# Kernel optimization log

Measured on AMD Instinct MI355X. Metric: run time of the kernel, lower is better.

## Reference

```python
import jax, jax.numpy as jnp
import numpy as np

EPS = 1e-6
R_DEPTH = 12   # CONFIG['max_recursion_depth']
STACK = 48     # CONFIG['stack_size']
GB, CG, CC = 0.8, 2.0, 0.25  # graph_bias_scale, context_gate_strength, commitment_cost


def _g(k, shape, s=0.05):
    return (jax.random.normal(k, shape) * s).astype(jnp.float32)


def setup_inputs():
    D, V, B, S = 128, 16384, 32, 128
    NS, NM = 64, 128
    ks = iter(jax.random.split(jax.random.key(0), 40))
    return {
        "input_ids": jax.random.randint(next(ks), (B, S), 0, V),
        "prev_syn_idx": jax.random.randint(next(ks), (B,), 0, NS),
        "prev_sem_idx": jax.random.randint(next(ks), (B,), 0, NM),
        "emb_mag": _g(next(ks), (V, D), 1.0),
        "emb_phase": _g(next(ks), (V, D), 1.0),
        "cell_Wr": _g(next(ks), (D, D)), "cell_Wi": _g(next(ks), (D, D)),
        "norm_scale": jnp.ones((D,), jnp.float32),
        "norm_shift": jnp.zeros((D,), jnp.float32),
        "modrelu_b": jnp.zeros((D,), jnp.float32),
        "qWr": _g(next(ks), (D, D)), "qWi": _g(next(ks), (D, D)),
        "kWr": _g(next(ks), (D, D)), "kWi": _g(next(ks), (D, D)),
        "vWr": _g(next(ks), (D, D)), "vWi": _g(next(ks), (D, D)),
        "oWr": _g(next(ks), (D, D)), "oWi": _g(next(ks), (D, D)),
        "halt_W": _g(next(ks), (2 * D, 1)),
        "halt_b": jnp.full((1,), -2.0, jnp.float32),  # nn.init.constant_(halt_linear.bias, -2.0)
        "stk_W": _g(next(ks), (2 * D, 3)), "stk_b": jnp.zeros((3,), jnp.float32),
        "cb_syn": _g(next(ks), (64, 2 * D), 1.0),
        "cb_sem": _g(next(ks), (128, 2 * D), 1.0),
        "ctxsyn_W": _g(next(ks), (2 * D, NS)), "ctxsyn_b": jnp.zeros((NS,), jnp.float32),
        "ctxsem_W": _g(next(ks), (2 * D, NM)), "ctxsem_b": jnp.zeros((NM,), jnp.float32),
        "adj_syn": _g(next(ks), (NS, NS), 1.0),
        "adj_sem": _g(next(ks), (NM, NM), 1.0),
        "gate_W": _g(next(ks), (4 * D, D)), "gate_b": jnp.zeros((D,), jnp.float32),
        "dec_W": _g(next(ks), (2 * D, V)), "dec_b": jnp.zeros((V,), jnp.float32),
    }


def _forward(fl, input_ids, prev_syn_idx, prev_sem_idx):
    (emb_mag, emb_phase, cell_Wr, cell_Wi, norm_scale, norm_shift, modrelu_b,
     qWr, qWi, kWr, kWi, vWr, vWi, oWr, oWi, halt_W, halt_b, stk_W, stk_b,
     cb_syn, cb_sem, ctxsyn_W, ctxsyn_b, ctxsem_W, ctxsem_b, adj_syn, adj_sem,
     gate_W, gate_b, dec_W, dec_b) = fl
    B = input_ids.shape[0]
    D = emb_mag.shape[1]
    sg = jax.lax.stop_gradient

    def clin(r, i, Wr, Wi):  # ComplexLinear (no bias)
        return r @ Wr - i @ Wi, i @ Wr + r @ Wi

    def cell(zr, zi):  # AdaptiveRecursiveCell
        r, i = clin(zr, zi, cell_Wr, cell_Wi)
        # ComplexLayerNorm (torch.var is unbiased -> ddof=1)
        mag = jnp.sqrt(r * r + i * i) + EPS
        mean = mag.mean(-1, keepdims=True)
        var = jnp.var(mag, axis=-1, ddof=1, keepdims=True)
        nm = (mag - mean) / jnp.sqrt(var + EPS) * norm_scale + norm_shift
        r, i = nm * r / mag, nm * i / mag  # cos/sin of original phase
        # ModReLU
        n = jnp.sqrt(r * r + i * i) + EPS
        s = jax.nn.relu(n + modrelu_b) / n
        r, i = r * s, i * s
        # MultiHeadComplexAttention: source computes Q,K but out = V -> o_proj(v_proj(z))
        vr, vi = clin(r, i, vWr, vWi)
        r, i = clin(vr, vi, oWr, oWi)
        zf = jnp.concatenate([r, i], -1)
        halt = jax.nn.sigmoid(zf @ halt_W + halt_b)          # [B,1]
        ctrl = jax.nn.softmax(zf @ stk_W + stk_b, axis=-1)   # [B,3]
        return r, i, halt, ctrl

    def stack_step(zr, zi, mem, ptr, ctrl):  # DifferentiableStack
        push, pop, noop = ctrl[:, 0:1], ctrl[:, 1:2], ctrl[:, 2:3]
        pu, pd = jnp.roll(ptr, 1, axis=1), jnp.roll(ptr, -1, axis=1)
        nptr = push * pu + pop * pd + noop * ptr
        nptr = nptr / (nptr.sum(1, keepdims=True) + EPS)
        zf = jnp.concatenate([zr, zi], -1)
        wm = (push * pu)[:, :, None]                          # write mask [B,STACK,1]
        mem = wm * zf[:, None, :] + mem * (1.0 - wm)
        read = (mem * nptr[:, :, None]).sum(1)                # [B,2D]
        return read[:, :D], read[:, D:], mem, nptr

    def gres(zr, zi, sr, si):  # GatedResidual, g_c = g + i*g
        g = jax.nn.sigmoid(jnp.concatenate([zr, zi, sr, si], -1) @ gate_W + gate_b)
        return ((1.0 - g) * zr + g * zi + g * (sr - si),
                (1.0 - g) * zi - g * zr + g * (si + sr))

    def vq(zr, zi, cb, adj, cW, cbias, pidx):  # ContextAwareDualVQ.vq_step (eval mode)
        zf = jnp.concatenate([zr, zi], -1)                    # [B,2D]
        d = (zf * zf).sum(1, keepdims=True) + (cb * cb).sum(1) - 2.0 * zf @ cb.T
        d = d - GB * jax.nn.sigmoid(adj[pidx]) - CG * jax.nn.softmax(zf @ cW + cbias, -1)
        idx = jnp.argmin(d, axis=1)
        zq = cb[idx]
        loss = jnp.mean((sg(zq) - zf) ** 2) + CC * jnp.mean((zq - sg(zf)) ** 2)
        return zf + sg(zq - zf), loss, idx                    # STE

    def step(carry, ids_t):
        mem, ptr, psyn, psem, lacc = carry
        r, th = emb_mag[ids_t], emb_phase[ids_t]              # embed
        zr, zi = r * jnp.cos(th), r * jnp.sin(th)
        rem = jnp.ones((B, 1), zr.dtype)
        accr = jnp.zeros_like(zr); acci = jnp.zeros_like(zi)
        slr = jnp.zeros_like(zr); sli = jnp.zeros_like(zi)
        for n in range(R_DEPTH):  # ACT recursion, halting-weighted accumulation
            pr, pi, halt, ctrl = cell(zr, zi)
            rr, ri, mem, ptr = stack_step(pr, pi, mem, ptr, ctrl)
            zr, zi = gres(pr, pi, rr, ri)
            w = rem if n == R_DEPTH - 1 else rem * halt
            accr, acci = accr + w * zr, acci + w * zi
            rem = rem * (1.0 - halt)
            slr, sli = slr + zr / R_DEPTH, sli + zi / R_DEPTH
        zqs, ls, isyn = vq(accr, acci, cb_syn, adj_syn, ctxsyn_W, ctxsyn_b, psyn)
        zqm, lm, isem = vq(slr, sli, cb_sem, adj_sem, ctxsem_W, ctxsem_b, psem)
        logits = 0.5 * (zqs + zqm) @ dec_W + dec_b            # decoder: Linear(2D, V)
        return (mem, ptr, isyn, isem, lacc + ls + lm), logits

    mem0 = jnp.zeros((B, STACK, 2 * D), jnp.float32)
    ptr0 = jnp.zeros((B, STACK), jnp.float32).at[:, 0].set(1.0)
    carry0 = (mem0, ptr0, prev_syn_idx, prev_sem_idx, jnp.zeros((), jnp.float32))
    (_, _, _, _, vq_loss), logits = jax.lax.scan(step, carry0, input_ids.T)
    return jnp.transpose(logits, (1, 0, 2)), vq_loss          # [B,S,V], scalar


def reference(input_ids, prev_syn_idx, prev_sem_idx, emb_mag, emb_phase, cell_Wr, cell_Wi, norm_scale, norm_shift, modrelu_b, qWr, qWi, kWr, kWi, vWr, vWi, oWr, oWi, halt_W, halt_b, stk_W, stk_b, cb_syn, cb_sem, ctxsyn_W, ctxsyn_b, ctxsem_W, ctxsem_b, adj_syn, adj_sem, gate_W, gate_b, dec_W, dec_b):
    fl = (emb_mag, emb_phase, cell_Wr, cell_Wi, norm_scale, norm_shift, modrelu_b,
          qWr, qWi, kWr, kWi, vWr, vWi, oWr, oWi, halt_W, halt_b, stk_W, stk_b,
          cb_syn, cb_sem, ctxsyn_W, ctxsyn_b, ctxsem_W, ctxsem_b, adj_syn, adj_sem,
          gate_W, gate_b, dec_W, dec_b)
    return _forward(fl, input_ids, prev_syn_idx, prev_sem_idx)
```

## Files before the change

kernel.cpp:

```cpp
#include <hip/hip_runtime.h>
#include <math.h>

#define D 128
#define D2 256
#define STK 48
#define SEQ 128
#define BATCH 32
#define RDPT 12
#define NSYN 64
#define NSEM 128
#define VOC 16384
#define EPSF 1e-6f
#define GB_C 0.8f
#define CG_C 2.0f

struct RParams {
  const int* input_ids;
  const int* prev_syn;
  const int* prev_sem;
  const float* emb_mag;
  const float* emb_phase;
  const float* cell_Wr;
  const float* cell_Wi;
  const float* norm_scale;
  const float* norm_shift;
  const float* modrelu_b;
  const float* VOr;
  const float* VOi;
  const float* halt_W;
  const float* halt_b;
  const float* stk_W;
  const float* stk_b;
  const float* cb_syn;
  const float* cb_sem;
  const float* ctxsyn_W;
  const float* ctxsyn_b;
  const float* ctxsem_W;
  const float* ctxsem_b;
  const float* gate_W;
  const float* gate_b;
  const float* cbT_syn;
  const float* cbT_sem;
  const float* cnrm_syn;
  const float* cnrm_sem;
  const float* gbsig_syn;
  const float* gbsig_sem;
  float* X;
  float* lossp;
};

__device__ __forceinline__ float waveAllSum(float v) {
  #pragma unroll
  for (int m = 32; m; m >>= 1) v += __shfl_xor(v, m);
  return v;
}

__global__ __launch_bounds__(512, 2) void recur_kernel(RParams p) {
  __shared__ float4 VO4[(D / 2) * D];
  __shared__ float partr[512], parti[512];
  __shared__ alignas(16) float xr_[D], xi_[D], cr_[D], ci_[D];
  __shared__ alignas(16) float zfc[D2], rd_[D2];
  __shared__ alignas(16) float acc2[D2], sl2[D2];
  __shared__ float zqs[D2];
  __shared__ float sptr[STK];
  __shared__ alignas(16) float nptrs[STK], wms[STK];
  __shared__ float sns_s[D], nsh_s[D], smb_s[D];
  __shared__ float hW_s[D2];
  __shared__ float stW_s[D2 * 3];
  __shared__ float scal[16];
  __shared__ int icb[2];
  __shared__ int ids[SEQ];

  const int tid = threadIdx.x;
  const int b = blockIdx.x;
  const int l = tid & 63;
  const int j = tid & 127;
  const int kq = tid >> 7;
  const int k0 = kq * 32;

  float cwr[32], cwi[32];
  #pragma unroll
  for (int kk = 0; kk < 32; ++kk) {
    cwr[kk] = p.cell_Wr[(size_t)(k0 + kk) * D + j];
    cwi[kk] = p.cell_Wi[(size_t)(k0 + kk) * D + j];
  }
  float gw[128];
  #pragma unroll
  for (int kk = 0; kk < 128; ++kk)
    gw[kk] = p.gate_W[(size_t)(kq * 128 + kk) * D + j];
  for (int e = tid; e < (D / 2) * D; e += 512) {
    const int kp = e >> 7;
    const int jj = e & 127;
    float4 w;
    w.x = p.VOr[(size_t)(2 * kp) * D + jj];
    w.y = p.VOi[(size_t)(2 * kp) * D + jj];
    w.z = p.VOr[(size_t)(2 * kp + 1) * D + jj];
    w.w = p.VOi[(size_t)(2 * kp + 1) * D + jj];
    VO4[e] = w;
  }
  if (tid < D) {
    sns_s[tid] = p.norm_scale[tid];
    nsh_s[tid] = p.norm_shift[tid];
    smb_s[tid] = p.modrelu_b[tid];
  }
  const float sgbR = (tid < D) ? p.gate_b[tid] : 0.f;
  if (tid < D2) hW_s[tid] = p.halt_W[tid];
  for (int e = tid; e < D2 * 3; e += 512) stW_s[e] = p.stk_W[e];
  if (tid < SEQ) ids[tid] = p.input_ids[(size_t)b * SEQ + tid];
  if (tid < STK) sptr[tid] = (tid == 0) ? 1.f : 0.f;
  if (tid == 0) { icb[0] = p.prev_syn[b]; icb[1] = p.prev_sem[b]; }
  const float hb = p.halt_b[0];
  const float sb0 = p.stk_b[0], sb1 = p.stk_b[1], sb2 = p.stk_b[2];

  float memv[24];
  #pragma unroll
  for (int q = 0; q < 24; ++q) memv[q] = 0.f;
  const int mdl = tid & 255, mjh = tid >> 8;
  float lossAcc = 0.f;
  float remv = 1.f;
  float mNxt = 0.f, pNxt = 0.f;
  __syncthreads();

  if (tid < D) {
    const int id0 = ids[0];
    mNxt = p.emb_mag[(size_t)id0 * D + tid];
    pNxt = p.emb_phase[(size_t)id0 * D + tid];
  }

  for (int t = 0; t < SEQ; ++t) {
    if (tid < D) {
      float sv, cv;
      sincosf(pNxt, &sv, &cv);
      xr_[tid] = mNxt * cv;
      xi_[tid] = mNxt * sv;
    }
    float accR = 0.f, accI = 0.f, slR = 0.f, slI = 0.f;
    if (tid < 64) remv = 1.f;
    __syncthreads();

    for (int n = 0; n < RDPT; ++n) {
      {
        const float4* x4r = (const float4*)(&xr_[k0]);
        const float4* x4i = (const float4*)(&xi_[k0]);
        float a0 = 0.f, a1 = 0.f, a2 = 0.f, a3 = 0.f;
        #pragma unroll
        for (int q = 0; q < 8; ++q) {
          float4 xa = x4r[q];
          float4 xb = x4i[q];
          a0 = fmaf(xa.x, cwr[q*4+0], a0); a0 = fmaf(-xb.x, cwi[q*4+0], a0);
          a1 = fmaf(xb.x, cwr[q*4+0], a1); a1 = fmaf(xa.x, cwi[q*4+0], a1);
          a2 = fmaf(xa.y, cwr[q*4+1], a2); a2 = fmaf(-xb.y, cwi[q*4+1], a2);
          a3 = fmaf(xb.y, cwr[q*4+1], a3); a3 = fmaf(xa.y, cwi[q*4+1], a3);
          a0 = fmaf(xa.z, cwr[q*4+2], a0); a0 = fmaf(-xb.z, cwi[q*4+2], a0);
          a1 = fmaf(xb.z, cwr[q*4+2], a1); a1 = fmaf(xa.z, cwi[q*4+2], a1);
          a2 = fmaf(xa.w, cwr[q*4+3], a2); a2 = fmaf(-xb.w, cwi[q*4+3], a2);
          a3 = fmaf(xb.w, cwr[q*4+3], a3); a3 = fmaf(xa.w, cwi[q*4+3], a3);
        }
        partr[tid] = a0 + a2;
        parti[tid] = a1 + a3;
      }
      __syncthreads();
      if (tid < 64) {
        float rr0 = 0.f, ii0 = 0.f, rr1 = 0.f, ii1 = 0.f;
        #pragma unroll
        for (int q = 0; q < 4; ++q) {
          rr0 += partr[l + q * 128];       ii0 += parti[l + q * 128];
          rr1 += partr[l + 64 + q * 128];  ii1 += parti[l + 64 + q * 128];
        }
        float m0 = sqrtf(rr0 * rr0 + ii0 * ii0) + EPSF;
        float m1 = sqrtf(rr1 * rr1 + ii1 * ii1) + EPSF;
        float mean = waveAllSum(m0 + m1) * (1.f / D);
        float dd0 = m0 - mean, dd1 = m1 - mean;
        float istd = rsqrtf(waveAllSum(dd0 * dd0 + dd1 * dd1) * (1.f / (D - 1)) + EPSF);
        float nm0 = (m0 - mean) * istd * sns_s[l] + nsh_s[l];
        float r0_ = nm0 * rr0 / m0, i0_ = nm0 * ii0 / m0;
        float nn0 = sqrtf(r0_ * r0_ + i0_ * i0_) + EPSF;
        float sc0 = fmaxf(nn0 + smb_s[l], 0.f) / nn0;
        cr_[l] = r0_ * sc0;
        ci_[l] = i0_ * sc0;
        float nm1 = (m1 - mean) * istd * sns_s[l + 64] + nsh_s[l + 64];
        float r1_ = nm1 * rr1 / m1, i1_ = nm1 * ii1 / m1;
        float nn1 = sqrtf(r1_ * r1_ + i1_ * i1_) + EPSF;
        float sc1 = fmaxf(nn1 + smb_s[l + 64], 0.f) / nn1;
        cr_[l + 64] = r1_ * sc1;
        ci_[l + 64] = i1_ * sc1;
      }
      __syncthreads();
      {
        const float4* c4r = (const float4*)(&cr_[k0]);
        const float4* c4i = (const float4*)(&ci_[k0]);
        const float4* vbase = &VO4[(size_t)(k0 >> 1) * D + j];
        float a0 = 0.f, a1 = 0.f, a2 = 0.f, a3 = 0.f;
        #pragma unroll
        for (int q = 0; q < 8; ++q) {
          float4 xa = c4r[q];
          float4 xb = c4i[q];
          float4 wA = vbase[(size_t)(2 * q) * D];
          float4 wB = vbase[(size_t)(2 * q + 1) * D];
          a0 = fmaf(xa.x, wA.x, a0); a0 = fmaf(-xb.x, wA.y, a0);
          a1 = fmaf(xb.x, wA.x, a1); a1 = fmaf(xa.x, wA.y, a1);
          a2 = fmaf(xa.y, wA.z, a2); a2 = fmaf(-xb.y, wA.w, a2);
          a3 = fmaf(xb.y, wA.z, a3); a3 = fmaf(xa.y, wA.w, a3);
          a0 = fmaf(xa.z, wB.x, a0); a0 = fmaf(-xb.z, wB.y, a0);
          a1 = fmaf(xb.z, wB.x, a1); a1 = fmaf(xa.z, wB.y, a1);
          a2 = fmaf(xa.w, wB.z, a2); a2 = fmaf(-xb.w, wB.w, a2);
          a3 = fmaf(xb.w, wB.z, a3); a3 = fmaf(xa.w, wB.w, a3);
        }
        partr[tid] = a0 + a2;
        parti[tid] = a1 + a3;
      }
      __syncthreads();
      if (tid < 256) {
        if (tid < 128) {
          zfc[tid] = partr[tid] + partr[tid + 128] + partr[tid + 256] + partr[tid + 384];
        } else {
          const int d = tid - 128;
          zfc[tid] = parti[d] + parti[d + 128] + parti[d + 256] + parti[d + 384];
        }
      }
      __syncthreads();
      if (tid < 64) {
        float z0 = zfc[l], z1 = zfc[l + 64], z2 = zfc[l + 128], z3 = zfc[l + 192];
        float dh  = z0 * hW_s[l] + z1 * hW_s[l + 64] + z2 * hW_s[l + 128] + z3 * hW_s[l + 192];
        float dc0 = z0 * stW_s[l * 3 + 0] + z1 * stW_s[(l + 64) * 3 + 0] +
                    z2 * stW_s[(l + 128) * 3 + 0] + z3 * stW_s[(l + 192) * 3 + 0];
        float dc1 = z0 * stW_s[l * 3 + 1] + z1 * stW_s[(l + 64) * 3 + 1] +
                    z2 * stW_s[(l + 128) * 3 + 1] + z3 * stW_s[(l + 192) * 3 + 1];
        float dc2 = z0 * stW_s[l * 3 + 2] + z1 * stW_s[(l + 64) * 3 + 2] +
                    z2 * stW_s[(l + 128) * 3 + 2] + z3 * stW_s[(l + 192) * 3 + 2];
        dh = waveAllSum(dh);
        dc0 = waveAllSum(dc0);
        dc1 = waveAllSum(dc1);
        dc2 = waveAllSum(dc2);
        float halt = 1.f / (1.f + expf(-(dh + hb)));
        float e0 = dc0 + sb0, e1 = dc1 + sb1, e2 = dc2 + sb2;
        float mx = fmaxf(e0, fmaxf(e1, e2));
        float x0 = expf(e0 - mx), x1 = expf(e1 - mx), x2 = expf(e2 - mx);
        float sm = x0 + x1 + x2;
        float push = x0 / sm, pop = x1 / sm, noop = x2 / sm;
        float wgt = (n == RDPT - 1) ? remv : remv * halt;
        if (l == 0) scal[3] = wgt;
        remv = remv * (1.f - halt);
        float pj = 0.f, pu = 0.f, pd = 0.f;
        if (l < STK) {
          pj = sptr[l];
          pu = sptr[(l + STK - 1) % STK];
          pd = sptr[(l + 1) % STK];
        }
        float np_ = push * pu + pop * pd + noop * pj;
        float wm_ = push * pu;
        float ssum = waveAllSum((l < STK) ? np_ : 0.f);
        float inv = 1.f / (ssum + EPSF);
        if (l < STK) {
          np_ *= inv;
          nptrs[l] = np_;
          sptr[l] = np_;
          wms[l] = wm_;
        }
      }
      __syncthreads();
      {
        const float4* wm4 = (const float4*)wms;
        const float4* np4 = (const float4*)nptrs;
        float zfd = zfc[mdl];
        float accA = 0.f, accB = 0.f;
        #pragma unroll
        for (int m4 = 0; m4 < 6; ++m4) {
          float4 wmv = wm4[mjh * 6 + m4];
          float4 npv = np4[mjh * 6 + m4];
          const int base = m4 * 4;
          memv[base + 0] = wmv.x * zfd + memv[base + 0] * (1.f - wmv.x);
          accA = fmaf(memv[base + 0], npv.x, accA);
          memv[base + 1] = wmv.y * zfd + memv[base + 1] * (1.f - wmv.y);
          accB = fmaf(memv[base + 1], npv.y, accB);
          memv[base + 2] = wmv.z * zfd + memv[base + 2] * (1.f - wmv.z);
          accA = fmaf(memv[base + 2], npv.z, accA);
          memv[base + 3] = wmv.w * zfd + memv[base + 3] * (1.f - wmv.w);
          accB = fmaf(memv[base + 3], npv.w, accB);
        }
        partr[tid] = accA + accB;
      }
      __syncthreads();
      if (tid < D2) rd_[tid] = partr[tid] + partr[tid + 256];
      __syncthreads();
      {
        const float4* src4 = (kq < 2) ? (const float4*)(&zfc[kq * 128])
                                      : (const float4*)(&rd_[(kq - 2) * 128]);
        float g0 = 0.f, g1 = 0.f, g2 = 0.f, g3 = 0.f;
        #pragma unroll
        for (int q = 0; q < 32; ++q) {
          float4 xv = src4[q];
          g0 = fmaf(xv.x, gw[q * 4 + 0], g0);
          g1 = fmaf(xv.y, gw[q * 4 + 1], g1);
          g2 = fmaf(xv.z, gw[q * 4 + 2], g2);
          g3 = fmaf(xv.w, gw[q * 4 + 3], g3);
        }
        partr[tid] = (g0 + g1) + (g2 + g3);
      }
      __syncthreads();
      if (tid < D) {
        float g = partr[tid] + partr[tid + 128] + partr[tid + 256] +
                  partr[tid + 384] + sgbR;
        g = 1.f / (1.f + expf(-g));
        float pr_ = zfc[tid], pi_ = zfc[tid + 128];
        float rr_ = rd_[tid], ri_ = rd_[tid + 128];
        float nzr = (1.f - g) * pr_ + g * pi_ + g * (rr_ - ri_);
        float nzi = (1.f - g) * pi_ - g * pr_ + g * (ri_ + rr_);
        xr_[tid] = nzr;
        xi_[tid] = nzi;
        float wgt = scal[3];
        accR += wgt * nzr;
        accI += wgt * nzi;
        slR += nzr * (1.f / RDPT);
        slI += nzi * (1.f / RDPT);
      }
      __syncthreads();
    }

    if (tid < D) {
      const int idn = ids[(t + 1 < SEQ) ? t + 1 : t];
      mNxt = p.emb_mag[(size_t)idn * D + tid];
      pNxt = p.emb_phase[(size_t)idn * D + tid];
    }
    if (tid < D) {
      acc2[tid] = accR; acc2[tid + 128] = accI;
      sl2[tid] = slR;  sl2[tid + 128] = slI;
    }
    __syncthreads();

    {
      const int c = tid & 63, ch = tid >> 6;
      const int kb = ch * 32;
      const float* cb = p.cbT_syn + (size_t)kb * 64 + c;
      const float* cw = p.ctxsyn_W + (size_t)kb * 64 + c;
      const float4* a4 = (const float4*)(&acc2[kb]);
      float d0 = 0.f, d1 = 0.f, e0 = 0.f, e1 = 0.f;
      #pragma unroll
      for (int q = 0; q < 8; ++q) {
        float4 zv = a4[q];
        d0 = fmaf(cb[(size_t)(q * 4 + 0) * 64], zv.x, d0);
        e0 = fmaf(cw[(size_t)(q * 4 + 0) * 64], zv.x, e0);
        d1 = fmaf(cb[(size_t)(q * 4 + 1) * 64], zv.y, d1);
        e1 = fmaf(cw[(size_t)(q * 4 + 1) * 64], zv.y, e1);
        d0 = fmaf(cb[(size_t)(q * 4 + 2) * 64], zv.z, d0);
        e0 = fmaf(cw[(size_t)(q * 4 + 2) * 64], zv.z, e0);
        d1 = fmaf(cb[(size_t)(q * 4 + 3) * 64], zv.w, d1);
        e1 = fmaf(cw[(size_t)(q * 4 + 3) * 64], zv.w, e1);
      }
      partr[ch * 64 + c] = d0 + d1;
      parti[ch * 64 + c] = e0 + e1;
    }
    __syncthreads();
    if (tid < 64) {
      float dot = 0.f, e = p.ctxsyn_b[l];
      #pragma unroll
      for (int ch = 0; ch < 8; ++ch) {
        dot += partr[ch * 64 + l];
        e += parti[ch * 64 + l];
      }
      float d = p.cnrm_syn[l] - 2.f * dot;
      float m = e;
      #pragma unroll
      for (int mm = 32; mm; mm >>= 1) m = fmaxf(m, __shfl_xor(m, mm));
      float ex = expf(e - m);
      float s = waveAllSum(ex);
      const int pidx = icb[0];
      float score = d - p.gbsig_syn[(size_t)pidx * 64 + l] - CG_C * (ex / s);
      float bv = score; int bi = l;
      #pragma unroll
      for (int mm = 32; mm; mm >>= 1) {
        float ov = __shfl_xor(bv, mm); int oi = __shfl_xor(bi, mm);
        if (ov < bv || (ov == bv && oi < bi)) { bv = ov; bi = oi; }
      }
      if (l == 0) icb[0] = bi;
    }
    __syncthreads();
    if (tid < D2) {
      const int idx = icb[0];
      float zqv = p.cb_syn[(size_t)idx * D2 + tid];
      float df = zqv - acc2[tid];
      lossAcc += df * df;
      zqs[tid] = zqv;
    }
    {
      const int c = tid & 127, ch = tid >> 7;
      const int kb = ch * 64;
      const float* cb = p.cbT_sem + (size_t)kb * 128 + c;
      const float* cw = p.ctxsem_W + (size_t)kb * 128 + c;
      const float4* a4 = (const float4*)(&sl2[kb]);
      float d0 = 0.f, d1 = 0.f, e0 = 0.f, e1 = 0.f;
      #pragma unroll
      for (int q = 0; q < 16; ++q) {
        float4 zv = a4[q];
        d0 = fmaf(cb[(size_t)(q * 4 + 0) * 128], zv.x, d0);
        e0 = fmaf(cw[(size_t)(q * 4 + 0) * 128], zv.x, e0);
        d1 = fmaf(cb[(size_t)(q * 4 + 1) * 128], zv.y, d1);
        e1 = fmaf(cw[(size_t)(q * 4 + 1) * 128], zv.y, e1);
        d0 = fmaf(cb[(size_t)(q * 4 + 2) * 128], zv.z, d0);
        e0 = fmaf(cw[(size_t)(q * 4 + 2) * 128], zv.z, e0);
        d1 = fmaf(cb[(size_t)(q * 4 + 3) * 128], zv.w, d1);
        e1 = fmaf(cw[(size_t)(q * 4 + 3) * 128], zv.w, e1);
      }
      partr[ch * 128 + c] = d0 + d1;
      parti[ch * 128 + c] = e0 + e1;
    }
    __syncthreads();
    if (tid < 64) {
      float dot0 = 0.f, e0 = p.ctxsem_b[l];
      float dot1 = 0.f, e1 = p.ctxsem_b[l + 64];
      #pragma unroll
      for (int ch = 0; ch < 4; ++ch) {
        dot0 += partr[ch * 128 + l];       e0 += parti[ch * 128 + l];
        dot1 += partr[ch * 128 + l + 64];  e1 += parti[ch * 128 + l + 64];
      }
      float d0 = p.cnrm_sem[l] - 2.f * dot0;
      float d1 = p.cnrm_sem[l + 64] - 2.f * dot1;
      float m = fmaxf(e0, e1);
      #pragma unroll
      for (int mm = 32; mm; mm >>= 1) m = fmaxf(m, __shfl_xor(m, mm));
      float x0 = expf(e0 - m), x1 = expf(e1 - m);
      float s = waveAllSum(x0 + x1);
      const int pidx = icb[1];
      float s0 = d0 - p.gbsig_sem[(size_t)pidx * 128 + l] - CG_C * (x0 / s);
      float s1 = d1 - p.gbsig_sem[(size_t)pidx * 128 + l + 64] - CG_C * (x1 / s);
      float bv = s0; int bi = l;
      if (s1 < bv) { bv = s1; bi = l + 64; }
      #pragma unroll
      for (int mm = 32; mm; mm >>= 1) {
        float ov = __shfl_xor(bv, mm); int oi = __shfl_xor(bi, mm);
        if (ov < bv || (ov == bv && oi < bi)) { bv = ov; bi = oi; }
      }
      if (l == 0) icb[1] = bi;
    }
    __syncthreads();
    if (tid < D2) {
      const int idx = icb[1];
      float zqv = p.cb_sem[(size_t)idx * D2 + tid];
      float df = zqv - sl2[tid];
      lossAcc += df * df;
      p.X[(size_t)(b * SEQ + t) * D2 + tid] = 0.5f * (zqs[tid] + zqv);
    }
    __syncthreads();
  }

  partr[tid] = lossAcc;
  __syncthreads();
  if (tid < 256) partr[tid] += partr[tid + 256];
  __syncthreads();
  if (tid < 128) partr[tid] += partr[tid + 128];
  __syncthreads();
  if (tid < 64) {
    float v = partr[tid] + partr[tid + 64];
    v = waveAllSum(v);
    if (tid == 0) p.lossp[b] = v;
  }
}

__global__ __launch_bounds__(256) void voprod_kernel(const float* __restrict__ vr,
                                                     const float* __restrict__ vi,
                                                     const float* __restrict__ orr,
                                                     const float* __restrict__ oii,
                                                     float* __restrict__ VOr,
                                                     float* __restrict__ VOi) {
  __shared__ float a_r[D], a_i[D];
  const int k = blockIdx.x;
  const int tid = threadIdx.x;
  if (tid < D) { a_r[tid] = vr[k * D + tid]; a_i[tid] = vi[k * D + tid]; }
  __syncthreads();
  const int m = tid & 127;
  const int half = tid >> 7;
  float acc = 0.f;
  if (half == 0) {
    #pragma unroll 8
    for (int jj = 0; jj < D; ++jj)
      acc += a_r[jj] * orr[jj * D + m] - a_i[jj] * oii[jj * D + m];
    VOr[k * D + m] = acc;
  } else {
    #pragma unroll 8
    for (int jj = 0; jj < D; ++jj)
      acc += a_r[jj] * oii[jj * D + m] + a_i[jj] * orr[jj * D + m];
    VOi[k * D + m] = acc;
  }
}

__global__ void vqprep_kernel(const float* __restrict__ cb_syn,
                              const float* __restrict__ cb_sem,
                              const float* __restrict__ adj_syn,
                              const float* __restrict__ adj_sem,
                              float* __restrict__ cbT_syn,
                              float* __restrict__ cbT_sem,
                              float* __restrict__ cnrm_syn,
                              float* __restrict__ cnrm_sem,
                              float* __restrict__ gbsig_syn,
                              float* __restrict__ gbsig_sem) {
  const int tid = blockIdx.x * 256 + threadIdx.x;
  const int nt = gridDim.x * 256;
  for (int e = tid; e < NSYN * D2; e += nt) {
    int c = e / D2, k = e % D2;
    cbT_syn[k * NSYN + c] = cb_syn[e];
  }
  for (int e = tid; e < NSEM * D2; e += nt) {
    int c = e / D2, k = e % D2;
    cbT_sem[k * NSEM + c] = cb_sem[e];
  }
  for (int c = tid; c < NSYN; c += nt) {
    float s = 0.f;
    for (int k = 0; k < D2; ++k) { float v = cb_syn[c * D2 + k]; s += v * v; }
    cnrm_syn[c] = s;
  }
  for (int c = tid; c < NSEM; c += nt) {
    float s = 0.f;
    for (int k = 0; k < D2; ++k) { float v = cb_sem[c * D2 + k]; s += v * v; }
    cnrm_sem[c] = s;
  }
  for (int e = tid; e < NSYN * NSYN; e += nt)
    gbsig_syn[e] = GB_C / (1.f + expf(-adj_syn[e]));
  for (int e = tid; e < NSEM * NSEM; e += nt)
    gbsig_sem[e] = GB_C / (1.f + expf(-adj_sem[e]));
}

__global__ __launch_bounds__(256) void dec_kernel(const float* __restrict__ X,
                                                  const float* __restrict__ W,
                                                  const float* __restrict__ bias,
                                                  float* __restrict__ out) {
  __shared__ float A[32][D2];
  const int tid = threadIdx.x;
  const int bx = blockIdx.x;
  const int by = blockIdx.y;
  const float* xr = X + (size_t)by * 32 * D2;
  #pragma unroll
  for (int s = 0; s < 32; ++s) A[s][tid] = xr[s * D2 + tid];
  __syncthreads();
  const int ty = tid >> 5, tx = tid & 31;
  const int col0 = bx * 128 + tx * 4;
  const int r0 = ty * 4;
  float acc[4][4];
  #pragma unroll
  for (int r = 0; r < 4; ++r) {
    acc[r][0] = 0.f; acc[r][1] = 0.f; acc[r][2] = 0.f; acc[r][3] = 0.f;
  }
  const float* wp = W + col0;
  for (int k = 0; k < D2; k += 4) {
    float4 w0 = *(const float4*)(wp + (size_t)(k + 0) * VOC);
    float4 w1 = *(const float4*)(wp + (size_t)(k + 1) * VOC);
    float4 w2 = *(const float4*)(wp + (size_t)(k + 2) * VOC);
    float4 w3 = *(const float4*)(wp + (size_t)(k + 3) * VOC);
    #pragma unroll
    for (int r = 0; r < 4; ++r) {
      float4 a = *(const float4*)&A[r0 + r][k];
      acc[r][0] += a.x * w0.x + a.y * w1.x + a.z * w2.x + a.w * w3.x;
      acc[r][1] += a.x * w0.y + a.y * w1.y + a.z * w2.y + a.w * w3.y;
      acc[r][2] += a.x * w0.z + a.y * w1.z + a.z * w2.z + a.w * w3.z;
      acc[r][3] += a.x * w0.w + a.y * w1.w + a.z * w2.w + a.w * w3.w;
    }
  }
  float4 bv = *(const float4*)(bias + col0);
  #pragma unroll
  for (int r = 0; r < 4; ++r) {
    float4 o;
    o.x = acc[r][0] + bv.x; o.y = acc[r][1] + bv.y;
    o.z = acc[r][2] + bv.z; o.w = acc[r][3] + bv.w;
    *(float4*)(out + (size_t)(by * 32 + r0 + r) * VOC + col0) = o;
  }
}

__global__ void loss_kernel(const float* __restrict__ lp, float* __restrict__ out) {
  int l = threadIdx.x;
  float v = (l < BATCH) ? lp[l] : 0.f;
  #pragma unroll
  for (int off = 32; off; off >>= 1) v += __shfl_down(v, off);
  if (l == 0) out[0] = v * (1.25f / 8192.f);
}

extern "C" void kernel_launch(void* const* d_in, const int* in_sizes, int n_in,
                              void* d_out, int out_size, void* d_ws,
                              size_t ws_size, hipStream_t stream) {
  float* ws = (float*)d_ws;
  float* X = ws;
  float* lossp = X + 1048576;
  float* VOr = lossp + 64;
  float* VOi = VOr + 16384;
  float* cbT_syn = VOi + 16384;
  float* cbT_sem = cbT_syn + 16384;
  float* cnrm_syn = cbT_sem + 32768;
  float* cnrm_sem = cnrm_syn + 64;
  float* gbsig_syn = cnrm_sem + 128;
  float* gbsig_sem = gbsig_syn + 4096;

  RParams p;
  p.input_ids  = (const int*)d_in[0];
  p.prev_syn   = (const int*)d_in[1];
  p.prev_sem   = (const int*)d_in[2];
  p.emb_mag    = (const float*)d_in[3];
  p.emb_phase  = (const float*)d_in[4];
  p.cell_Wr    = (const float*)d_in[5];
  p.cell_Wi    = (const float*)d_in[6];
  p.norm_scale = (const float*)d_in[7];
  p.norm_shift = (const float*)d_in[8];
  p.modrelu_b  = (const float*)d_in[9];
  p.VOr        = VOr;
  p.VOi        = VOi;
  p.halt_W     = (const float*)d_in[18];
  p.halt_b     = (const float*)d_in[19];
  p.stk_W      = (const float*)d_in[20];
  p.stk_b      = (const float*)d_in[21];
  p.cb_syn     = (const float*)d_in[22];
  p.cb_sem     = (const float*)d_in[23];
  p.ctxsyn_W   = (const float*)d_in[24];
  p.ctxsyn_b   = (const float*)d_in[25];
  p.ctxsem_W   = (const float*)d_in[26];
  p.ctxsem_b   = (const float*)d_in[27];
  p.gate_W     = (const float*)d_in[30];
  p.gate_b     = (const float*)d_in[31];
  const float* dec_W = (const float*)d_in[32];
  const float* dec_b = (const float*)d_in[33];
  p.cbT_syn = cbT_syn;
  p.cbT_sem = cbT_sem;
  p.cnrm_syn = cnrm_syn;
  p.cnrm_sem = cnrm_sem;
  p.gbsig_syn = gbsig_syn;
  p.gbsig_sem = gbsig_sem;
  p.X = X;
  p.lossp = lossp;

  float* out = (float*)d_out;

  voprod_kernel<<<D, 256, 0, stream>>>((const float*)d_in[14], (const float*)d_in[15],
                                       (const float*)d_in[16], (const float*)d_in[17],
                                       VOr, VOi);
  vqprep_kernel<<<64, 256, 0, stream>>>((const float*)d_in[22], (const float*)d_in[23],
                                        (const float*)d_in[28], (const float*)d_in[29],
                                        cbT_syn, cbT_sem, cnrm_syn, cnrm_sem,
                                        gbsig_syn, gbsig_sem);
  recur_kernel<<<BATCH, 512, 0, stream>>>(p);
  dec_kernel<<<dim3(VOC / 128, BATCH * SEQ / 32), 256, 0, stream>>>(X, dec_W,
                                                                    dec_b, out);
  loss_kernel<<<1, 64, 0, stream>>>(lossp, out + (size_t)BATCH * SEQ * VOC);
}
```

Measured before the change: 18.01 ms.

## Spread serial single-wave reductions in recurrence step across more waves

The post-matmul normalization and the halt/stack-control dot products were computed by a single 64-lane wave. They now use 128 threads and four waves, with partial results passed through shared memory and extra block barriers. Norm parameters move from shared memory into registers, and launch bounds drop the min-2-blocks hint. The aim is to shorten the serial critical path of each recursion step, at the cost of more __syncthreads per step and possibly different register allocation.

Result: no change. 18.20 ms (+1.0%).

```diff
diff --git a/kernel.cpp b/kernel.cpp
--- a/kernel.cpp
+++ b/kernel.cpp
@@ -55,16 +55,16 @@
   return v;
 }
 
-__global__ __launch_bounds__(512, 2) void recur_kernel(RParams p) {
+__global__ __launch_bounds__(512) void recur_kernel(RParams p) {
   __shared__ float4 VO4[(D / 2) * D];
   __shared__ float partr[512], parti[512];
   __shared__ alignas(16) float xr_[D], xi_[D], cr_[D], ci_[D];
+  __shared__ float rAiA[D2], marr[D];
   __shared__ alignas(16) float zfc[D2], rd_[D2];
   __shared__ alignas(16) float acc2[D2], sl2[D2];
   __shared__ float zqs[D2];
   __shared__ float sptr[STK];
   __shared__ alignas(16) float nptrs[STK], wms[STK];
-  __shared__ float sns_s[D], nsh_s[D], smb_s[D];
   __shared__ float hW_s[D2];
   __shared__ float stW_s[D2 * 3];
   __shared__ float scal[16];
@@ -73,6 +73,7 @@
 
   const int tid = threadIdx.x;
   const int b = blockIdx.x;
+  const int wv = tid >> 6;
   const int l = tid & 63;
   const int j = tid & 127;
   const int kq = tid >> 7;
@@ -98,12 +99,13 @@
     w.w = p.VOi[(size_t)(2 * kp + 1) * D + jj];
     VO4[e] = w;
   }
+  float snsR = 0.f, nshR = 0.f, smbR = 0.f, sgbR = 0.f;
   if (tid < D) {
-    sns_s[tid] = p.norm_scale[tid];
-    nsh_s[tid] = p.norm_shift[tid];
-    smb_s[tid] = p.modrelu_b[tid];
-  }
-  const float sgbR = (tid < D) ? p.gate_b[tid] : 0.f;
+    snsR = p.norm_scale[tid];
+    nshR = p.norm_shift[tid];
+    smbR = p.modrelu_b[tid];
+    sgbR = p.gate_b[tid];
+  }
   if (tid < D2) hW_s[tid] = p.halt_W[tid];
   for (int e = tid; e < D2 * 3; e += 512) stW_s[e] = p.stk_W[e];
   if (tid < SEQ) ids[tid] = p.input_ids[(size_t)b * SEQ + tid];
@@ -160,30 +162,34 @@
         parti[tid] = a1 + a3;
       }
       __syncthreads();
+      if (tid < D) {
+        float rr = partr[tid] + partr[tid + 128] + partr[tid + 256] + partr[tid + 384];
+        float ii = parti[tid] + parti[tid + 128] + parti[tid + 256] + parti[tid + 384];
+        rAiA[tid] = rr;
+        rAiA[tid + 128] = ii;
+        marr[tid] = sqrtf(rr * rr + ii * ii) + EPSF;
+      }
+      __syncthreads();
       if (tid < 64) {
-        float rr0 = 0.f, ii0 = 0.f, rr1 = 0.f, ii1 = 0.f;
-        #pragma unroll
-        for (int q = 0; q < 4; ++q) {
-          rr0 += partr[l + q * 128];       ii0 += parti[l + q * 128];
-          rr1 += partr[l + 64 + q * 128];  ii1 += parti[l + 64 + q * 128];
-        }
-        float m0 = sqrtf(rr0 * rr0 + ii0 * ii0) + EPSF;
-        float m1 = sqrtf(rr1 * rr1 + ii1 * ii1) + EPSF;
+        float m0 = marr[l], m1 = marr[l + 64];
         float mean = waveAllSum(m0 + m1) * (1.f / D);
-        float dd0 = m0 - mean, dd1 = m1 - mean;
-        float istd = rsqrtf(waveAllSum(dd0 * dd0 + dd1 * dd1) * (1.f / (D - 1)) + EPSF);
-        float nm0 = (m0 - mean) * istd * sns_s[l] + nsh_s[l];
-        float r0_ = nm0 * rr0 / m0, i0_ = nm0 * ii0 / m0;
-        float nn0 = sqrtf(r0_ * r0_ + i0_ * i0_) + EPSF;
-        float sc0 = fmaxf(nn0 + smb_s[l], 0.f) / nn0;
-        cr_[l] = r0_ * sc0;
-        ci_[l] = i0_ * sc0;
-        float nm1 = (m1 - mean) * istd * sns_s[l + 64] + nsh_s[l + 64];
-        float r1_ = nm1 * rr1 / m1, i1_ = nm1 * ii1 / m1;
-        float nn1 = sqrtf(r1_ * r1_ + i1_ * i1_) + EPSF;
-        float sc1 = fmaxf(nn1 + smb_s[l + 64], 0.f) / nn1;
-        cr_[l + 64] = r1_ * sc1;
-        ci_[l + 64] = i1_ * sc1;
+        float d0 = m0 - mean, d1 = m1 - mean;
+        float v = waveAllSum(d0 * d0 + d1 * d1);
+        if (l == 0) {
+          scal[1] = mean;
+          scal[2] = rsqrtf(v * (1.f / (D - 1)) + EPSF);
+        }
+      }
+      __syncthreads();
+      if (tid < D) {
+        float m = marr[tid];
+        float nm = (m - scal[1]) * scal[2] * snsR + nshR;
+        float r_ = nm * rAiA[tid] / m;
+        float i_ = nm * rAiA[tid + 128] / m;
+        float nn = sqrtf(r_ * r_ + i_ * i_) + EPSF;
+        float sc = fmaxf(nn + smbR, 0.f) / nn;
+        cr_[tid] = r_ * sc;
+        ci_[tid] = i_ * sc;
       }
       __syncthreads();
       {
@@ -219,21 +225,23 @@
         }
       }
       __syncthreads();
+      if (tid < 256) {
+        float z0 = zfc[l], z1 = zfc[l + 64], z2 = zfc[l + 128], z3 = zfc[l + 192];
+        float s;
+        if (wv == 0) {
+          s = z0 * hW_s[l] + z1 * hW_s[l + 64] + z2 * hW_s[l + 128] + z3 * hW_s[l + 192];
+        } else {
+          const int c = wv - 1;
+          s = z0 * stW_s[l * 3 + c] + z1 * stW_s[(l + 64) * 3 + c] +
+              z2 * stW_s[(l + 128) * 3 + c] + z3 * stW_s[(l + 192) * 3 + c];
+        }
+        s = waveAllSum(s);
+        if (l == 0) scal[4 + wv] = s;
+      }
+      __syncthreads();
       if (tid < 64) {
-        float z0 = zfc[l], z1 = zfc[l + 64], z2 = zfc[l + 128], z3 = zfc[l + 192];
-        float dh  = z0 * hW_s[l] + z1 * hW_s[l + 64] + z2 * hW_s[l + 128] + z3 * hW_s[l + 192];
-        float dc0 = z0 * stW_s[l * 3 + 0] + z1 * stW_s[(l + 64) * 3 + 0] +
-                    z2 * stW_s[(l + 128) * 3 + 0] + z3 * stW_s[(l + 192) * 3 + 0];
-        float dc1 = z0 * stW_s[l * 3 + 1] + z1 * stW_s[(l + 64) * 3 + 1] +
-                    z2 * stW_s[(l + 128) * 3 + 1] + z3 * stW_s[(l + 192) * 3 + 1];
-        float dc2 = z0 * stW_s[l * 3 + 2] + z1 * stW_s[(l + 64) * 3 + 2] +
-                    z2 * stW_s[(l + 128) * 3 + 2] + z3 * stW_s[(l + 192) * 3 + 2];
-        dh = waveAllSum(dh);
-        dc0 = waveAllSum(dc0);
-        dc1 = waveAllSum(dc1);
-        dc2 = waveAllSum(dc2);
-        float halt = 1.f / (1.f + expf(-(dh + hb)));
-        float e0 = dc0 + sb0, e1 = dc1 + sb1, e2 = dc2 + sb2;
+        float halt = 1.f / (1.f + expf(-(scal[4] + hb)));
+        float e0 = scal[5] + sb0, e1 = scal[6] + sb1, e2 = scal[7] + sb2;
         float mx = fmaxf(e0, fmaxf(e1, e2));
         float x0 = expf(e0 - mx), x1 = expf(e1 - mx), x2 = expf(e2 - mx);
         float sm = x0 + x1 + x2;
```
